# Kernel optimization log

Hardware: AMD Instinct MI355X
Metric: run time of the kernel (lower is better)

Reference implementation:

```python
import jax, jax.numpy as jnp
import numpy as np

HEAD_SIZE = 64
EMBED_DIM = 1024

def setup_inputs() -> dict:
    key = jax.random.key(0)
    kx, kq, kk, kv = jax.random.split(key, 4)
    B, T, C, H = 8, 2048, EMBED_DIM, HEAD_SIZE
    scale = 1.0 / np.sqrt(C)
    x = jax.random.normal(kx, (B, T, C), dtype=jnp.float32)
    # nn.Linear(C, H, bias=False): weight (H, C); store as (C, H) for x @ W
    Wq = jax.random.normal(kq, (C, H), dtype=jnp.float32) * scale
    Wk = jax.random.normal(kk, (C, H), dtype=jnp.float32) * scale
    Wv = jax.random.normal(kv, (C, H), dtype=jnp.float32) * scale
    return {"x": x, "Wq": Wq, "Wk": Wk, "Wv": Wv}

def reference(x, Wq, Wk, Wv):
    B, T, C = x.shape
    H = Wq.shape[1]
    q = x @ Wq  # (B, T, H)
    k = x @ Wk
    v = x @ Wv
    # scaled scores with causal mask (tril)
    wei = jnp.einsum('bth,bsh->bts', q, k) * (H ** -0.5)  # (B, T, T)
    causal = jnp.tril(jnp.ones((T, T), dtype=bool))
    wei = jnp.where(causal, wei, -jnp.inf)
    wei = jax.nn.softmax(wei, axis=-1)
    out = jnp.einsum('bts,bsh->bth', wei, v)  # (B, T, H)
    return out
```

## Files before the change

kernel.cpp:

```cpp
#include <hip/hip_runtime.h>

#define T_SEQ 2048
#define C_DIM 1024
#define H_DIM 64
#define B_DIM 8
#define NROW (B_DIM * T_SEQ)

typedef __attribute__((ext_vector_type(8))) short short8;
typedef __attribute__((ext_vector_type(4))) float f32x4;

__device__ __forceinline__ short f2bf(float f) {
  unsigned u = __builtin_bit_cast(unsigned, f);
  u += 0x7fffu + ((u >> 16) & 1u);
  return (short)(u >> 16);
}

__global__ __launch_bounds__(256) void w_prep(
    const float* __restrict__ Wq, const float* __restrict__ Wk,
    const float* __restrict__ Wv, short* __restrict__ Wt2) {
  const int unit = blockIdx.x * 256 + threadIdx.x;
  const int lane = unit & 63;
  const int t = unit >> 6;
  const int kh = t & 3;
  const int g = t >> 2;
  const int ntg = g % 12;
  const int kc = g / 12;
  const int n16 = lane & 15, quad = lane >> 4;
  const int mat = ntg >> 2;
  const int h = (ntg & 3) * 16 + n16;
  const int kb = kc * 128 + kh * 32 + quad * 8;
  const float* W = (mat == 0) ? Wq : (mat == 1 ? Wk : Wv);
  short8 v;
#pragma unroll
  for (int e = 0; e < 8; ++e) v[e] = f2bf(W[(size_t)(kb + e) * H_DIM + h]);
  *(short8*)(Wt2 + (size_t)unit * 8) = v;
}

__device__ __forceinline__ int lds_addr(int tile, int kh, int qd, int nn) {
  return tile * 2048 + kh * 512 + (qd * 16 + (nn ^ ((kh * 4 + qd) & 7))) * 8;
}

__global__ __launch_bounds__(256, 2) void qkv_gemm(
    const float* __restrict__ x, const short* __restrict__ Wt2,
    short* __restrict__ q, short* __restrict__ k, short* __restrict__ vt) {
  __shared__ __align__(16) short As[2][4096];
  const int tid = threadIdx.x;
  const int w = tid >> 6, lane = tid & 63;
  const int n16 = lane & 15, quad = lane >> 4;
  const int row0 = blockIdx.x * 32;

  f32x4 acc[2][3];
#pragma unroll
  for (int mt = 0; mt < 2; ++mt)
#pragma unroll
    for (int ln = 0; ln < 3; ++ln) acc[mt][ln] = (f32x4){0.f, 0.f, 0.f, 0.f};

  const int u20 = tid, u21 = 256 + tid;
  const int sr0 = u20 >> 4, f0 = u20 & 15;
  const int sr1 = u21 >> 4, f1 = u21 & 15;
  const float* ap0 = x + (size_t)(row0 + sr0) * C_DIM + f0 * 8;
  const float* ap1 = x + (size_t)(row0 + sr1) * C_DIM + f1 * 8;
  const int soff0 = lds_addr(sr0 >> 4, f0 >> 2, f0 & 3, sr0 & 15);
  const int soff1 = lds_addr(sr1 >> 4, f1 >> 2, f1 & 3, sr1 & 15);

  int swz[4];
#pragma unroll
  for (int kh = 0; kh < 4; ++kh)
    swz[kh] = (quad * 16 + (n16 ^ ((kh * 4 + quad) & 7))) * 8;

  const short* bbase = Wt2 + (size_t)(w * 3) * 2048 + (size_t)lane * 8;

  float4 astg[2][4];
  short8 bfr[12];

#define STAGE_A(d, p)                                      \
  {                                                        \
    short8 av0, av1;                                       \
    _Pragma("unroll") for (int e = 0; e < 4; ++e) {        \
      av0[e] = f2bf(((const float*)&astg[d][0])[e]);       \
      av0[e + 4] = f2bf(((const float*)&astg[d][1])[e]);   \
      av1[e] = f2bf(((const float*)&astg[d][2])[e]);       \
      av1[e + 4] = f2bf(((const float*)&astg[d][3])[e]);   \
    }                                                      \
    *(short8*)(&As[p][0] + soff0) = av0;                   \
    *(short8*)(&As[p][0] + soff1) = av1;                   \
  }

  astg[0][0] = *(const float4*)(ap0);
  astg[0][1] = *(const float4*)(ap0 + 4);
  astg[0][2] = *(const float4*)(ap1);
  astg[0][3] = *(const float4*)(ap1 + 4);
  astg[1][0] = *(const float4*)(ap0 + 128);
  astg[1][1] = *(const float4*)(ap0 + 132);
  astg[1][2] = *(const float4*)(ap1 + 128);
  astg[1][3] = *(const float4*)(ap1 + 132);
#pragma unroll
  for (int ln = 0; ln < 3; ++ln)
#pragma unroll
    for (int kh = 0; kh < 4; ++kh)
      bfr[ln * 4 + kh] = *(const short8*)(bbase + ln * 2048 + kh * 512);
  STAGE_A(0, 0);
  asm volatile("s_waitcnt lgkmcnt(0)" ::: "memory");
  __builtin_amdgcn_sched_barrier(0);
  __builtin_amdgcn_s_barrier();
  __builtin_amdgcn_sched_barrier(0);

#pragma unroll
  for (int kc = 0; kc < 8; ++kc) {
    const short* asb = &As[kc & 1][0];
#pragma unroll
    for (int kh = 0; kh < 4; ++kh) {
      const short8 a0 = *(const short8*)(asb + kh * 512 + swz[kh]);
      const short8 a1 = *(const short8*)(asb + 2048 + kh * 512 + swz[kh]);
#pragma unroll
      for (int ln = 0; ln < 3; ++ln) {
        acc[0][ln] = __builtin_amdgcn_mfma_f32_16x16x32_bf16(
            a0, bfr[ln * 4 + kh], acc[0][ln], 0, 0, 0);
        acc[1][ln] = __builtin_amdgcn_mfma_f32_16x16x32_bf16(
            a1, bfr[ln * 4 + kh], acc[1][ln], 0, 0, 0);
      }
    }
    if (kc < 7) {
      const short* bc = bbase + (size_t)(kc + 1) * 24576;
#pragma unroll
      for (int ln = 0; ln < 3; ++ln)
#pragma unroll
        for (int kh = 0; kh < 4; ++kh)
          bfr[ln * 4 + kh] = *(const short8*)(bc + ln * 2048 + kh * 512);
      if (kc < 6) {
        astg[kc & 1][0] = *(const float4*)(ap0 + (kc + 2) * 128);
        astg[kc & 1][1] = *(const float4*)(ap0 + (kc + 2) * 128 + 4);
        astg[kc & 1][2] = *(const float4*)(ap1 + (kc + 2) * 128);
        astg[kc & 1][3] = *(const float4*)(ap1 + (kc + 2) * 128 + 4);
      }
      STAGE_A((kc + 1) & 1, (kc + 1) & 1);
      asm volatile("s_waitcnt lgkmcnt(0)" ::: "memory");
      __builtin_amdgcn_sched_barrier(0);
      __builtin_amdgcn_s_barrier();
      __builtin_amdgcn_sched_barrier(0);
    }
  }
#undef STAGE_A

  const int b = row0 >> 11;
#pragma unroll
  for (int mt = 0; mt < 2; ++mt)
#pragma unroll
    for (int ln = 0; ln < 3; ++ln) {
      const int ntg = w * 3 + ln;
      const int mat = ntg >> 2;
      const int cl = (ntg & 3) * 16 + n16;
#pragma unroll
      for (int r = 0; r < 4; ++r) {
        const int row = row0 + mt * 16 + quad * 4 + r;
        const float v = acc[mt][ln][r];
        if (mat == 0)
          q[(size_t)row * H_DIM + cl] = f2bf(v * 0.125f);
        else if (mat == 1)
          k[(size_t)row * H_DIM + cl] = f2bf(v);
        else
          vt[((size_t)b * H_DIM + cl) * T_SEQ + (row & (T_SEQ - 1))] = f2bf(v);
      }
    }
}

__global__ __launch_bounds__(256) void attn_mfma(
    const short* __restrict__ q, const short* __restrict__ k,
    const short* __restrict__ vt, float* __restrict__ out) {
  __shared__ __align__(16) short pbuf[4][2048];
  __shared__ __align__(16) float oshare[3][2048];
  __shared__ __align__(16) float lshare[3][512];
  const int tid = threadIdx.x;
  const int w = tid >> 6;
  const int lane = tid & 63;
  const int n16 = lane & 15, quad = lane >> 4;
  const int b = blockIdx.x & 7;
  const int pa = blockIdx.x >> 3;
  const int r0a = pa * 16;
  const int r0b = (127 - pa) * 16;

  const short* kb = k + (size_t)b * T_SEQ * H_DIM;
  const short* vb = vt + (size_t)b * H_DIM * T_SEQ;
  const short* qpa = q + ((size_t)b * T_SEQ + r0a) * H_DIM;
  const short* qpb = q + ((size_t)b * T_SEQ + r0b) * H_DIM;

  short8 aqA[2], aqB[2];
  aqA[0] = *(const short8*)(qpa + (size_t)n16 * H_DIM + quad * 8);
  aqA[1] = *(const short8*)(qpa + (size_t)n16 * H_DIM + 32 + quad * 8);
  aqB[0] = *(const short8*)(qpb + (size_t)n16 * H_DIM + quad * 8);
  aqB[1] = *(const short8*)(qpb + (size_t)n16 * H_DIM + 32 + quad * 8);

  f32x4 OA[4], OB[4];
#pragma unroll
  for (int i = 0; i < 4; ++i) {
    OA[i] = (f32x4){0.f, 0.f, 0.f, 0.f};
    OB[i] = (f32x4){0.f, 0.f, 0.f, 0.f};
  }
  float lsA[4] = {0.f, 0.f, 0.f, 0.f};
  float lsB[4] = {0.f, 0.f, 0.f, 0.f};

  const int nj = (r0b + 16 + 63) >> 6;
  const int njA = (r0a + 16 + 63) >> 6;

  for (int jt = w; jt < nj; jt += 4) {
    const int j0 = jt * 64;
    const bool actA = (jt < njA);

    short8 bk[4][2];
#pragma unroll
    for (int nt = 0; nt < 4; ++nt) {
      const short* kp = kb + (size_t)(j0 + nt * 16 + n16) * H_DIM + quad * 8;
      bk[nt][0] = *(const short8*)kp;
      bk[nt][1] = *(const short8*)(kp + 32);
    }

    f32x4 sB[4];
#pragma unroll
    for (int nt = 0; nt < 4; ++nt) {
      f32x4 z = (f32x4){0.f, 0.f, 0.f, 0.f};
      z = __builtin_amdgcn_mfma_f32_16x16x32_bf16(aqB[0], bk[nt][0], z, 0, 0, 0);
      z = __builtin_amdgcn_mfma_f32_16x16x32_bf16(aqB[1], bk[nt][1], z, 0, 0, 0);
      sB[nt] = z;
    }
    f32x4 sA[4];
    if (actA) {
#pragma unroll
      for (int nt = 0; nt < 4; ++nt) {
        f32x4 z = (f32x4){0.f, 0.f, 0.f, 0.f};
        z = __builtin_amdgcn_mfma_f32_16x16x32_bf16(aqA[0], bk[nt][0], z, 0, 0, 0);
        z = __builtin_amdgcn_mfma_f32_16x16x32_bf16(aqA[1], bk[nt][1], z, 0, 0, 0);
        sA[nt] = z;
      }
    }

    const bool fullB = (j0 + 64 <= r0b);
#pragma unroll
    for (int nt = 0; nt < 4; ++nt) {
      const int base =
          (nt >> 1) * 512 + ((((nt & 1) << 1) | (n16 >> 3)) * 128) + (n16 & 7);
#pragma unroll
      for (int r = 0; r < 4; ++r) {
        float p;
        if (fullB) {
          p = __expf(sB[nt][r]);
        } else {
          const int j = j0 + nt * 16 + n16;
          const int row = r0b + quad * 4 + r;
          p = (j <= row) ? __expf(sB[nt][r]) : 0.f;
        }
        lsB[r] += p;
        pbuf[w][1024 + base + (quad * 4 + r) * 8] = f2bf(p);
      }
    }
    if (actA) {
      const bool fullA = (j0 + 64 <= r0a);
#pragma unroll
      for (int nt = 0; nt < 4; ++nt) {
        const int base =
            (nt >> 1) * 512 + ((((nt & 1) << 1) | (n16 >> 3)) * 128) + (n16 & 7);
#pragma unroll
        for (int r = 0; r < 4; ++r) {
          float p;
          if (fullA) {
            p = __expf(sA[nt][r]);
          } else {
            const int j = j0 + nt * 16 + n16;
            const int row = r0a + quad * 4 + r;
            p = (j <= row) ? __expf(sA[nt][r]) : 0.f;
          }
          lsA[r] += p;
          pbuf[w][base + (quad * 4 + r) * 8] = f2bf(p);
        }
      }
    }

    short8 bv[4][2];
#pragma unroll
    for (int ht = 0; ht < 4; ++ht)
#pragma unroll
      for (int kh = 0; kh < 2; ++kh)
        bv[ht][kh] = *(const short8*)(vb + (size_t)(ht * 16 + n16) * T_SEQ +
                                      j0 + kh * 32 + quad * 8);

    const short8 apB0 = *(const short8*)(&pbuf[w][1024] + lane * 8);
    const short8 apB1 = *(const short8*)(&pbuf[w][1536] + lane * 8);
#pragma unroll
    for (int ht = 0; ht < 4; ++ht) {
      OB[ht] = __builtin_amdgcn_mfma_f32_16x16x32_bf16(apB0, bv[ht][0], OB[ht], 0, 0, 0);
      OB[ht] = __builtin_amdgcn_mfma_f32_16x16x32_bf16(apB1, bv[ht][1], OB[ht], 0, 0, 0);
    }
    if (actA) {
      const short8 apA0 = *(const short8*)(&pbuf[w][0] + lane * 8);
      const short8 apA1 = *(const short8*)(&pbuf[w][512] + lane * 8);
#pragma unroll
      for (int ht = 0; ht < 4; ++ht) {
        OA[ht] = __builtin_amdgcn_mfma_f32_16x16x32_bf16(apA0, bv[ht][0], OA[ht], 0, 0, 0);
        OA[ht] = __builtin_amdgcn_mfma_f32_16x16x32_bf16(apA1, bv[ht][1], OA[ht], 0, 0, 0);
      }
    }
  }

  if (w != 0) {
#pragma unroll
    for (int ht = 0; ht < 4; ++ht)
#pragma unroll
      for (int r = 0; r < 4; ++r) {
        oshare[w - 1][(ht * 4 + r) * 64 + lane] = OA[ht][r];
        oshare[w - 1][1024 + (ht * 4 + r) * 64 + lane] = OB[ht][r];
      }
#pragma unroll
    for (int r = 0; r < 4; ++r) {
      lshare[w - 1][r * 64 + lane] = lsA[r];
      lshare[w - 1][256 + r * 64 + lane] = lsB[r];
    }
  }
  __syncthreads();
  if (w == 0) {
#pragma unroll
    for (int ht = 0; ht < 4; ++ht)
#pragma unroll
      for (int r = 0; r < 4; ++r) {
        float a = OA[ht][r], bb = OB[ht][r];
#pragma unroll
        for (int ow = 0; ow < 3; ++ow) {
          a += oshare[ow][(ht * 4 + r) * 64 + lane];
          bb += oshare[ow][1024 + (ht * 4 + r) * 64 + lane];
        }
        OA[ht][r] = a;
        OB[ht][r] = bb;
      }
#pragma unroll
    for (int r = 0; r < 4; ++r) {
      float va = lsA[r], vb2 = lsB[r];
#pragma unroll
      for (int ow = 0; ow < 3; ++ow) {
        va += lshare[ow][r * 64 + lane];
        vb2 += lshare[ow][256 + r * 64 + lane];
      }
      va += __shfl_xor(va, 1);
      va += __shfl_xor(va, 2);
      va += __shfl_xor(va, 4);
      va += __shfl_xor(va, 8);
      vb2 += __shfl_xor(vb2, 1);
      vb2 += __shfl_xor(vb2, 2);
      vb2 += __shfl_xor(vb2, 4);
      vb2 += __shfl_xor(vb2, 8);
      lsA[r] = va;
      lsB[r] = vb2;
    }
#pragma unroll
    for (int ht = 0; ht < 4; ++ht)
#pragma unroll
      for (int r = 0; r < 4; ++r) {
        out[((size_t)b * T_SEQ + r0a + quad * 4 + r) * H_DIM + ht * 16 + n16] =
            OA[ht][r] / lsA[r];
        out[((size_t)b * T_SEQ + r0b + quad * 4 + r) * H_DIM + ht * 16 + n16] =
            OB[ht][r] / lsB[r];
      }
  }
}

extern "C" void kernel_launch(void* const* d_in, const int* in_sizes, int n_in,
                              void* d_out, int out_size, void* d_ws,
                              size_t ws_size, hipStream_t stream) {
  const float* x = (const float*)d_in[0];
  const float* Wq = (const float*)d_in[1];
  const float* Wk = (const float*)d_in[2];
  const float* Wv = (const float*)d_in[3];

  char* ws = (char*)d_ws;
  short* Wt = (short*)ws;
  short* q = (short*)(ws + 3 * 64 * 1024 * 2);
  short* kk = (short*)(ws + 3 * 64 * 1024 * 2 + 2097152);
  short* vt = (short*)(ws + 3 * 64 * 1024 * 2 + 2 * 2097152);

  w_prep<<<96, 256, 0, stream>>>(Wq, Wk, Wv, Wt);
  qkv_gemm<<<NROW / 32, 256, 0, stream>>>(x, Wt, q, kk, vt);
  attn_mfma<<<B_DIM * (T_SEQ / 32), 256, 0, stream>>>(q, kk, vt, (float*)d_out);
}
```

Measured before the change: 137.0 us.

## Double-buffer K/V register loads across key tiles in attention loop

Restructures the per-wave key-tile loop to prefetch the next tile's K and V fragments into a second register set while the current tile's QK MFMAs and softmax run. The loop is manually unrolled by two with ping-pong buffers, and launch_bounds now requests 2 blocks per CU. The aim is to hide global load latency behind compute. It doubles the register footprint for K/V fragments, which the occupancy hint may force into spills.

```diff
diff --git a/kernel.cpp b/kernel.cpp
--- a/kernel.cpp
+++ b/kernel.cpp
@@ -164,7 +164,7 @@
     }
 }
 
-__global__ __launch_bounds__(256) void attn_mfma(
+__global__ __launch_bounds__(256, 2) void attn_mfma(
     const short* __restrict__ q, const short* __restrict__ k,
     const short* __restrict__ vt, float* __restrict__ out) {
   __shared__ __align__(16) short pbuf[4][2048];
@@ -202,103 +202,115 @@
   const int nj = (r0b + 16 + 63) >> 6;
   const int njA = (r0a + 16 + 63) >> 6;
 
-  for (int jt = w; jt < nj; jt += 4) {
-    const int j0 = jt * 64;
-    const bool actA = (jt < njA);
-
-    short8 bk[4][2];
-#pragma unroll
-    for (int nt = 0; nt < 4; ++nt) {
-      const short* kp = kb + (size_t)(j0 + nt * 16 + n16) * H_DIM + quad * 8;
-      bk[nt][0] = *(const short8*)kp;
-      bk[nt][1] = *(const short8*)(kp + 32);
-    }
-
-    f32x4 sB[4];
-#pragma unroll
-    for (int nt = 0; nt < 4; ++nt) {
-      f32x4 z = (f32x4){0.f, 0.f, 0.f, 0.f};
-      z = __builtin_amdgcn_mfma_f32_16x16x32_bf16(aqB[0], bk[nt][0], z, 0, 0, 0);
-      z = __builtin_amdgcn_mfma_f32_16x16x32_bf16(aqB[1], bk[nt][1], z, 0, 0, 0);
-      sB[nt] = z;
-    }
-    f32x4 sA[4];
-    if (actA) {
-#pragma unroll
-      for (int nt = 0; nt < 4; ++nt) {
-        f32x4 z = (f32x4){0.f, 0.f, 0.f, 0.f};
-        z = __builtin_amdgcn_mfma_f32_16x16x32_bf16(aqA[0], bk[nt][0], z, 0, 0, 0);
-        z = __builtin_amdgcn_mfma_f32_16x16x32_bf16(aqA[1], bk[nt][1], z, 0, 0, 0);
-        sA[nt] = z;
-      }
-    }
-
-    const bool fullB = (j0 + 64 <= r0b);
-#pragma unroll
-    for (int nt = 0; nt < 4; ++nt) {
-      const int base =
-          (nt >> 1) * 512 + ((((nt & 1) << 1) | (n16 >> 3)) * 128) + (n16 & 7);
-#pragma unroll
-      for (int r = 0; r < 4; ++r) {
-        float p;
-        if (fullB) {
-          p = __expf(sB[nt][r]);
-        } else {
-          const int j = j0 + nt * 16 + n16;
-          const int row = r0b + quad * 4 + r;
-          p = (j <= row) ? __expf(sB[nt][r]) : 0.f;
-        }
-        lsB[r] += p;
-        pbuf[w][1024 + base + (quad * 4 + r) * 8] = f2bf(p);
-      }
-    }
-    if (actA) {
-      const bool fullA = (j0 + 64 <= r0a);
-#pragma unroll
-      for (int nt = 0; nt < 4; ++nt) {
-        const int base =
-            (nt >> 1) * 512 + ((((nt & 1) << 1) | (n16 >> 3)) * 128) + (n16 & 7);
-#pragma unroll
-        for (int r = 0; r < 4; ++r) {
-          float p;
-          if (fullA) {
-            p = __expf(sA[nt][r]);
-          } else {
-            const int j = j0 + nt * 16 + n16;
-            const int row = r0a + quad * 4 + r;
-            p = (j <= row) ? __expf(sA[nt][r]) : 0.f;
-          }
-          lsA[r] += p;
-          pbuf[w][base + (quad * 4 + r) * 8] = f2bf(p);
-        }
-      }
-    }
-
-    short8 bv[4][2];
-#pragma unroll
-    for (int ht = 0; ht < 4; ++ht)
-#pragma unroll
-      for (int kh = 0; kh < 2; ++kh)
-        bv[ht][kh] = *(const short8*)(vb + (size_t)(ht * 16 + n16) * T_SEQ +
-                                      j0 + kh * 32 + quad * 8);
-
-    const short8 apB0 = *(const short8*)(&pbuf[w][1024] + lane * 8);
-    const short8 apB1 = *(const short8*)(&pbuf[w][1536] + lane * 8);
-#pragma unroll
-    for (int ht = 0; ht < 4; ++ht) {
-      OB[ht] = __builtin_amdgcn_mfma_f32_16x16x32_bf16(apB0, bv[ht][0], OB[ht], 0, 0, 0);
-      OB[ht] = __builtin_amdgcn_mfma_f32_16x16x32_bf16(apB1, bv[ht][1], OB[ht], 0, 0, 0);
-    }
-    if (actA) {
-      const short8 apA0 = *(const short8*)(&pbuf[w][0] + lane * 8);
-      const short8 apA1 = *(const short8*)(&pbuf[w][512] + lane * 8);
-#pragma unroll
-      for (int ht = 0; ht < 4; ++ht) {
-        OA[ht] = __builtin_amdgcn_mfma_f32_16x16x32_bf16(apA0, bv[ht][0], OA[ht], 0, 0, 0);
-        OA[ht] = __builtin_amdgcn_mfma_f32_16x16x32_bf16(apA1, bv[ht][1], OA[ht], 0, 0, 0);
-      }
-    }
-  }
+  short8 bk0[4][2], bv0[4][2], bk1[4][2], bv1[4][2];
+
+#define LOADK(BK, J0)                                                        \
+  _Pragma("unroll") for (int nt = 0; nt < 4; ++nt) {                         \
+    const short* kp = kb + (size_t)((J0) + nt * 16 + n16) * H_DIM + quad * 8; \
+    BK[nt][0] = *(const short8*)kp;                                          \
+    BK[nt][1] = *(const short8*)(kp + 32);                                   \
+  }
+#define LOADV(BV, J0)                                                        \
+  _Pragma("unroll") for (int ht = 0; ht < 4; ++ht)                           \
+  _Pragma("unroll") for (int kh = 0; kh < 2; ++kh)                           \
+      BV[ht][kh] = *(const short8*)(vb + (size_t)(ht * 16 + n16) * T_SEQ +   \
+                                    (J0) + kh * 32 + quad * 8);
+
+#define DOITER(BK, BV, JT, ...)                                               \
+  {                                                                           \
+    const int j0 = (JT) * 64;                                                 \
+    const bool actA = ((JT) < njA);                                           \
+    f32x4 sB[4];                                                              \
+    _Pragma("unroll") for (int nt = 0; nt < 4; ++nt) {                        \
+      f32x4 z = (f32x4){0.f, 0.f, 0.f, 0.f};                                  \
+      z = __builtin_amdgcn_mfma_f32_16x16x32_bf16(aqB[0], BK[nt][0], z, 0, 0, 0); \
+      z = __builtin_amdgcn_mfma_f32_16x16x32_bf16(aqB[1], BK[nt][1], z, 0, 0, 0); \
+      sB[nt] = z;                                                             \
+    }                                                                         \
+    f32x4 sA[4];                                                              \
+    if (actA) {                                                               \
+      _Pragma("unroll") for (int nt = 0; nt < 4; ++nt) {                      \
+        f32x4 z = (f32x4){0.f, 0.f, 0.f, 0.f};                                \
+        z = __builtin_amdgcn_mfma_f32_16x16x32_bf16(aqA[0], BK[nt][0], z, 0, 0, 0); \
+        z = __builtin_amdgcn_mfma_f32_16x16x32_bf16(aqA[1], BK[nt][1], z, 0, 0, 0); \
+        sA[nt] = z;                                                           \
+      }                                                                       \
+    }                                                                         \
+    __VA_ARGS__     \
+    const bool fullB = (j0 + 64 <= r0b);                                      \
+    _Pragma("unroll") for (int nt = 0; nt < 4; ++nt) {                        \
+      const int base = (nt >> 1) * 512 +                                      \
+                       ((((nt & 1) << 1) | (n16 >> 3)) * 128) + (n16 & 7);    \
+      _Pragma("unroll") for (int r = 0; r < 4; ++r) {                         \
+        float p;                                                              \
+        if (fullB) {                                                          \
+          p = __expf(sB[nt][r]);                                              \
+        } else {                                                              \
+          const int j = j0 + nt * 16 + n16;                                   \
+          const int row = r0b + quad * 4 + r;                                 \
+          p = (j <= row) ? __expf(sB[nt][r]) : 0.f;                           \
+        }                                                                     \
+        lsB[r] += p;                                                          \
+        pbuf[w][1024 + base + (quad * 4 + r) * 8] = f2bf(p);                  \
+      }                                                                       \
+    }                                                                         \
+    if (actA) {                                                               \
+      const bool fullA = (j0 + 64 <= r0a);                                    \
+      _Pragma("unroll") for (int nt = 0; nt < 4; ++nt) {                      \
+        const int base = (nt >> 1) * 512 +                                    \
+                         ((((nt & 1) << 1) | (n16 >> 3)) * 128) + (n16 & 7);  \
+        _Pragma("unroll") for (int r = 0; r < 4; ++r) {                       \
+          float p;                                                            \
+          if (fullA) {                                                        \
+            p = __expf(sA[nt][r]);                                            \
+          } else {                                                            \
+            const int j = j0 + nt * 16 + n16;                                 \
+            const int row = r0a + quad * 4 + r;                               \
+            p = (j <= row) ? __expf(sA[nt][r]) : 0.f;                         \
+          }                                                                   \
+          lsA[r] += p;                                                        \
+          pbuf[w][base + (quad * 4 + r) * 8] = f2bf(p);                       \
+        }                                                                     \
+      }                                                                       \
+    }                                                                         \
+    const short8 apB0 = *(const short8*)(&pbuf[w][1024] + lane * 8);          \
+    const short8 apB1 = *(const short8*)(&pbuf[w][1536] + lane * 8);          \
+    _Pragma("unroll") for (int ht = 0; ht < 4; ++ht) {                        \
+      OB[ht] = __builtin_amdgcn_mfma_f32_16x16x32_bf16(apB0, BV[ht][0], OB[ht], 0, 0, 0); \
+      OB[ht] = __builtin_amdgcn_mfma_f32_16x16x32_bf16(apB1, BV[ht][1], OB[ht], 0, 0, 0); \
+    }                                                                         \
+    if (actA) {                                                               \
+      const short8 apA0 = *(const short8*)(&pbuf[w][0] + lane * 8);           \
+      const short8 apA1 = *(const short8*)(&pbuf[w][512] + lane * 8);         \
+      _Pragma("unroll") for (int ht = 0; ht < 4; ++ht) {                      \
+        OA[ht] = __builtin_amdgcn_mfma_f32_16x16x32_bf16(apA0, BV[ht][0], OA[ht], 0, 0, 0); \
+        OA[ht] = __builtin_amdgcn_mfma_f32_16x16x32_bf16(apA1, BV[ht][1], OA[ht], 0, 0, 0); \
+      }                                                                       \
+    }                                                                         \
+  }
+
+  {
+    const int j00 = w * 64;
+    LOADK(bk0, j00);
+    LOADV(bv0, j00);
+  }
+  for (int jt = w; jt < nj; jt += 8) {
+    const int jB = jt + 4;
+    DOITER(bk0, bv0, jt, if (jB < nj) {
+      LOADK(bk1, jB * 64);
+      LOADV(bv1, jB * 64);
+    })
+    if (jB < nj) {
+      const int jC = jt + 8;
+      DOITER(bk1, bv1, jB, if (jC < nj) {
+        LOADK(bk0, jC * 64);
+        LOADV(bv0, jC * 64);
+      })
+    }
+  }
+#undef DOITER
+#undef LOADK
+#undef LOADV
 
   if (w != 0) {
 #pragma unroll
```

Result: slower. 148.5 us (+8.4%).

## Split attention KV loop across single-wave blocks with global partial combine kernel

Applied to the files above, without the earlier changes.

Replaces the 4-wave attention block, which reduced partials through shared memory, with 64-thread blocks. Each block handles one of 6 strided KV phases for a query tile pair, and the launch grows to 3072 blocks. Unnormalized partial outputs and row sums go to a global workspace, and a new combine kernel sums them and normalizes. The aim is more parallelism and occupancy, and less shared memory and block-level sync. The cost is an extra kernel launch plus about 25 MB of partial-result writes and reads through global memory. The V loads are also moved earlier in the loop to overlap with the score MFMAs.

```diff
diff --git a/kernel.cpp b/kernel.cpp
--- a/kernel.cpp
+++ b/kernel.cpp
@@ -5,6 +5,7 @@
 #define H_DIM 64
 #define B_DIM 8
 #define NROW (B_DIM * T_SEQ)
+#define PH 6
 
 typedef __attribute__((ext_vector_type(8))) short short8;
 typedef __attribute__((ext_vector_type(4))) float f32x4;
@@ -164,18 +165,17 @@
     }
 }
 
-__global__ __launch_bounds__(256) void attn_mfma(
+__global__ __launch_bounds__(64, 3) void attn_part(
     const short* __restrict__ q, const short* __restrict__ k,
-    const short* __restrict__ vt, float* __restrict__ out) {
-  __shared__ __align__(16) short pbuf[4][2048];
-  __shared__ __align__(16) float oshare[3][2048];
-  __shared__ __align__(16) float lshare[3][512];
-  const int tid = threadIdx.x;
-  const int w = tid >> 6;
-  const int lane = tid & 63;
+    const short* __restrict__ vt, float* __restrict__ Opart,
+    float* __restrict__ lpart) {
+  __shared__ __align__(16) short pbuf[2048];
+  const int lane = threadIdx.x;
   const int n16 = lane & 15, quad = lane >> 4;
-  const int b = blockIdx.x & 7;
-  const int pa = blockIdx.x >> 3;
+  const int blk = blockIdx.x;
+  const int b = blk & 7;
+  const int ph = (blk >> 3) % PH;
+  const int pa = blk / (8 * PH);
   const int r0a = pa * 16;
   const int r0b = (127 - pa) * 16;
 
@@ -199,10 +199,10 @@
   float lsA[4] = {0.f, 0.f, 0.f, 0.f};
   float lsB[4] = {0.f, 0.f, 0.f, 0.f};
 
-  const int nj = (r0b + 16 + 63) >> 6;
-  const int njA = (r0a + 16 + 63) >> 6;
-
-  for (int jt = w; jt < nj; jt += 4) {
+  const int nj = (r0b + 79) >> 6;
+  const int njA = (r0a + 79) >> 6;
+
+  for (int jt = ph; jt < nj; jt += PH) {
     const int j0 = jt * 64;
     const bool actA = (jt < njA);
 
@@ -213,6 +213,13 @@
       bk[nt][0] = *(const short8*)kp;
       bk[nt][1] = *(const short8*)(kp + 32);
     }
+    short8 bv[4][2];
+#pragma unroll
+    for (int ht = 0; ht < 4; ++ht)
+#pragma unroll
+      for (int kh = 0; kh < 2; ++kh)
+        bv[ht][kh] = *(const short8*)(vb + (size_t)(ht * 16 + n16) * T_SEQ +
+                                      j0 + kh * 32 + quad * 8);
 
     f32x4 sB[4];
 #pragma unroll
@@ -222,17 +229,6 @@
       z = __builtin_amdgcn_mfma_f32_16x16x32_bf16(aqB[1], bk[nt][1], z, 0, 0, 0);
       sB[nt] = z;
     }
-    f32x4 sA[4];
-    if (actA) {
-#pragma unroll
-      for (int nt = 0; nt < 4; ++nt) {
-        f32x4 z = (f32x4){0.f, 0.f, 0.f, 0.f};
-        z = __builtin_amdgcn_mfma_f32_16x16x32_bf16(aqA[0], bk[nt][0], z, 0, 0, 0);
-        z = __builtin_amdgcn_mfma_f32_16x16x32_bf16(aqA[1], bk[nt][1], z, 0, 0, 0);
-        sA[nt] = z;
-      }
-    }
-
     const bool fullB = (j0 + 64 <= r0b);
 #pragma unroll
     for (int nt = 0; nt < 4; ++nt) {
@@ -249,10 +245,19 @@
           p = (j <= row) ? __expf(sB[nt][r]) : 0.f;
         }
         lsB[r] += p;
-        pbuf[w][1024 + base + (quad * 4 + r) * 8] = f2bf(p);
-      }
-    }
+        pbuf[1024 + base + (quad * 4 + r) * 8] = f2bf(p);
+      }
+    }
+
     if (actA) {
+      f32x4 sA[4];
+#pragma unroll
+      for (int nt = 0; nt < 4; ++nt) {
+        f32x4 z = (f32x4){0.f, 0.f, 0.f, 0.f};
+        z = __builtin_amdgcn_mfma_f32_16x16x32_bf16(aqA[0], bk[nt][0], z, 0, 0, 0);
+        z = __builtin_amdgcn_mfma_f32_16x16x32_bf16(aqA[1], bk[nt][1], z, 0, 0, 0);
+        sA[nt] = z;
+      }
       const bool fullA = (j0 + 64 <= r0a);
 #pragma unroll
       for (int nt = 0; nt < 4; ++nt) {
@@ -269,29 +274,21 @@
             p = (j <= row) ? __expf(sA[nt][r]) : 0.f;
           }
           lsA[r] += p;
-          pbuf[w][base + (quad * 4 + r) * 8] = f2bf(p);
+          pbuf[base + (quad * 4 + r) * 8] = f2bf(p);
         }
       }
     }
 
-    short8 bv[4][2];
-#pragma unroll
-    for (int ht = 0; ht < 4; ++ht)
-#pragma unroll
-      for (int kh = 0; kh < 2; ++kh)
-        bv[ht][kh] = *(const short8*)(vb + (size_t)(ht * 16 + n16) * T_SEQ +
-                                      j0 + kh * 32 + quad * 8);
-
-    const short8 apB0 = *(const short8*)(&pbuf[w][1024] + lane * 8);
-    const short8 apB1 = *(const short8*)(&pbuf[w][1536] + lane * 8);
+    const short8 apB0 = *(const short8*)(&pbuf[1024] + lane * 8);
+    const short8 apB1 = *(const short8*)(&pbuf[1536] + lane * 8);
 #pragma unroll
     for (int ht = 0; ht < 4; ++ht) {
       OB[ht] = __builtin_amdgcn_mfma_f32_16x16x32_bf16(apB0, bv[ht][0], OB[ht], 0, 0, 0);
       OB[ht] = __builtin_amdgcn_mfma_f32_16x16x32_bf16(apB1, bv[ht][1], OB[ht], 0, 0, 0);
     }
     if (actA) {
-      const short8 apA0 = *(const short8*)(&pbuf[w][0] + lane * 8);
-      const short8 apA1 = *(const short8*)(&pbuf[w][512] + lane * 8);
+      const short8 apA0 = *(const short8*)(&pbuf[0] + lane * 8);
+      const short8 apA1 = *(const short8*)(&pbuf[512] + lane * 8);
 #pragma unroll
       for (int ht = 0; ht < 4; ++ht) {
         OA[ht] = __builtin_amdgcn_mfma_f32_16x16x32_bf16(apA0, bv[ht][0], OA[ht], 0, 0, 0);
@@ -300,63 +297,75 @@
     }
   }
 
-  if (w != 0) {
-#pragma unroll
-    for (int ht = 0; ht < 4; ++ht)
-#pragma unroll
-      for (int r = 0; r < 4; ++r) {
-        oshare[w - 1][(ht * 4 + r) * 64 + lane] = OA[ht][r];
-        oshare[w - 1][1024 + (ht * 4 + r) * 64 + lane] = OB[ht][r];
-      }
+#pragma unroll
+  for (int r = 0; r < 4; ++r) {
+    float va = lsA[r], vb2 = lsB[r];
+    va += __shfl_xor(va, 1);
+    va += __shfl_xor(va, 2);
+    va += __shfl_xor(va, 4);
+    va += __shfl_xor(va, 8);
+    vb2 += __shfl_xor(vb2, 1);
+    vb2 += __shfl_xor(vb2, 2);
+    vb2 += __shfl_xor(vb2, 4);
+    vb2 += __shfl_xor(vb2, 8);
+    lsA[r] = va;
+    lsB[r] = vb2;
+  }
+
+  float* opA = Opart + (size_t)blk * 2048;
+  float* opB = opA + 1024;
+#pragma unroll
+  for (int ht = 0; ht < 4; ++ht)
 #pragma unroll
     for (int r = 0; r < 4; ++r) {
-      lshare[w - 1][r * 64 + lane] = lsA[r];
-      lshare[w - 1][256 + r * 64 + lane] = lsB[r];
-    }
-  }
-  __syncthreads();
-  if (w == 0) {
-#pragma unroll
-    for (int ht = 0; ht < 4; ++ht)
-#pragma unroll
-      for (int r = 0; r < 4; ++r) {
-        float a = OA[ht][r], bb = OB[ht][r];
-#pragma unroll
-        for (int ow = 0; ow < 3; ++ow) {
-          a += oshare[ow][(ht * 4 + r) * 64 + lane];
-          bb += oshare[ow][1024 + (ht * 4 + r) * 64 + lane];
-        }
-        OA[ht][r] = a;
-        OB[ht][r] = bb;
-      }
+      opA[(ht * 4 + r) * 64 + lane] = OA[ht][r];
+      opB[(ht * 4 + r) * 64 + lane] = OB[ht][r];
+    }
+  if (n16 == 0) {
 #pragma unroll
     for (int r = 0; r < 4; ++r) {
-      float va = lsA[r], vb2 = lsB[r];
-#pragma unroll
-      for (int ow = 0; ow < 3; ++ow) {
-        va += lshare[ow][r * 64 + lane];
-        vb2 += lshare[ow][256 + r * 64 + lane];
-      }
-      va += __shfl_xor(va, 1);
-      va += __shfl_xor(va, 2);
-      va += __shfl_xor(va, 4);
-      va += __shfl_xor(va, 8);
-      vb2 += __shfl_xor(vb2, 1);
-      vb2 += __shfl_xor(vb2, 2);
-      vb2 += __shfl_xor(vb2, 4);
-      vb2 += __shfl_xor(vb2, 8);
-      lsA[r] = va;
-      lsB[r] = vb2;
-    }
-#pragma unroll
-    for (int ht = 0; ht < 4; ++ht)
-#pragma unroll
-      for (int r = 0; r < 4; ++r) {
-        out[((size_t)b * T_SEQ + r0a + quad * 4 + r) * H_DIM + ht * 16 + n16] =
-            OA[ht][r] / lsA[r];
-        out[((size_t)b * T_SEQ + r0b + quad * 4 + r) * H_DIM + ht * 16 + n16] =
-            OB[ht][r] / lsB[r];
-      }
+      lpart[blk * 32 + quad * 4 + r] = lsA[r];
+      lpart[blk * 32 + 16 + quad * 4 + r] = lsB[r];
+    }
+  }
+}
+
+__global__ __launch_bounds__(128) void attn_comb(
+    const float* __restrict__ Opart, const float* __restrict__ lpart,
+    float* __restrict__ out) {
+  const int tid = threadIdx.x;
+  const int lane = tid & 63;
+  const int half = tid >> 6;
+  const int n16 = lane & 15, quad = lane >> 4;
+  const int blk = blockIdx.x;
+  const int b = blk & 7;
+  const int tile = (blk >> 3) & 1;
+  const int pa = blk >> 4;
+  const int qt = tile ? (127 - pa) : pa;
+  const int r0 = qt * 16;
+
+  float acc[8];
+#pragma unroll
+  for (int u = 0; u < 8; ++u) acc[u] = 0.f;
+  float ls[4] = {0.f, 0.f, 0.f, 0.f};
+
+#pragma unroll
+  for (int p2 = 0; p2 < PH; ++p2) {
+    const int pblk = (pa * PH + p2) * 8 + b;
+    const float* op =
+        Opart + (size_t)pblk * 2048 + tile * 1024 + half * 512;
+#pragma unroll
+    for (int u = 0; u < 8; ++u) acc[u] += op[u * 64 + lane];
+    const float* lp = lpart + pblk * 32 + tile * 16;
+#pragma unroll
+    for (int r = 0; r < 4; ++r) ls[r] += lp[quad * 4 + r];
+  }
+
+#pragma unroll
+  for (int u = 0; u < 8; ++u) {
+    const int ht = half * 2 + (u >> 2), r = u & 3;
+    out[((size_t)b * T_SEQ + r0 + quad * 4 + r) * H_DIM + ht * 16 + n16] =
+        acc[u] / ls[r];
   }
 }
 
@@ -370,11 +379,14 @@
 
   char* ws = (char*)d_ws;
   short* Wt = (short*)ws;
-  short* q = (short*)(ws + 3 * 64 * 1024 * 2);
-  short* kk = (short*)(ws + 3 * 64 * 1024 * 2 + 2097152);
-  short* vt = (short*)(ws + 3 * 64 * 1024 * 2 + 2 * 2097152);
+  short* q = (short*)(ws + 393216);
+  short* kk = (short*)(ws + 393216 + 2097152);
+  short* vt = (short*)(ws + 393216 + 2 * 2097152);
+  float* Opart = (float*)(ws + 6684672);
+  float* lpart = (float*)(ws + 6684672 + 25165824);
 
   w_prep<<<96, 256, 0, stream>>>(Wq, Wk, Wv, Wt);
   qkv_gemm<<<NROW / 32, 256, 0, stream>>>(x, Wt, q, kk, vt);
-  attn_mfma<<<B_DIM * (T_SEQ / 32), 256, 0, stream>>>(q, kk, vt, (float*)d_out);
-}
+  attn_part<<<64 * PH * 8, 64, 0, stream>>>(q, kk, vt, Opart, lpart);
+  attn_comb<<<64 * 2 * 8, 128, 0, stream>>>(Opart, lpart, (float*)d_out);
+}
```

New measurement: 143.3 us. 1.05x slower.

## Transpose S MFMA and pass P through cross-lane shuffles instead of LDS

Applied to the files above, without the earlier changes.

The QK^T MFMA operands are swapped, so each lane holds score values along the key dimension for one query row. The exponentiated probabilities are packed to bf16 with v_cvt_pk_bf16_f32 and rearranged into the PV A-operand layout with __shfl_xor exchanges, which removes the per-wave LDS P buffer and its scattered 2-byte stores. Row sums are now kept as one per-lane scalar and redistributed with shuffles at the end. This cuts LDS traffic and frees shared memory, at the cost of extra shuffle and select instructions in the inner loop. The tricky lane-permutation logic is a correctness risk.

```diff
diff --git a/kernel.cpp b/kernel.cpp
--- a/kernel.cpp
+++ b/kernel.cpp
@@ -8,11 +8,18 @@
 
 typedef __attribute__((ext_vector_type(8))) short short8;
 typedef __attribute__((ext_vector_type(4))) float f32x4;
+typedef __attribute__((ext_vector_type(4))) int i32x4;
 
 __device__ __forceinline__ short f2bf(float f) {
   unsigned u = __builtin_bit_cast(unsigned, f);
   u += 0x7fffu + ((u >> 16) & 1u);
   return (short)(u >> 16);
+}
+
+__device__ __forceinline__ unsigned pk_bf16(float lo, float hi) {
+  unsigned r;
+  asm("v_cvt_pk_bf16_f32 %0, %1, %2" : "=v"(r) : "v"(lo), "v"(hi));
+  return r;
 }
 
 __global__ __launch_bounds__(256) void w_prep(
@@ -167,7 +174,6 @@
 __global__ __launch_bounds__(256) void attn_mfma(
     const short* __restrict__ q, const short* __restrict__ k,
     const short* __restrict__ vt, float* __restrict__ out) {
-  __shared__ __align__(16) short pbuf[4][2048];
   __shared__ __align__(16) float oshare[3][2048];
   __shared__ __align__(16) float lshare[3][512];
   const int tid = threadIdx.x;
@@ -196,8 +202,7 @@
     OA[i] = (f32x4){0.f, 0.f, 0.f, 0.f};
     OB[i] = (f32x4){0.f, 0.f, 0.f, 0.f};
   }
-  float lsA[4] = {0.f, 0.f, 0.f, 0.f};
-  float lsB[4] = {0.f, 0.f, 0.f, 0.f};
+  float lsAsc = 0.f, lsBsc = 0.f;
 
   const int nj = (r0b + 16 + 63) >> 6;
   const int njA = (r0a + 16 + 63) >> 6;
@@ -218,8 +223,8 @@
 #pragma unroll
     for (int nt = 0; nt < 4; ++nt) {
       f32x4 z = (f32x4){0.f, 0.f, 0.f, 0.f};
-      z = __builtin_amdgcn_mfma_f32_16x16x32_bf16(aqB[0], bk[nt][0], z, 0, 0, 0);
-      z = __builtin_amdgcn_mfma_f32_16x16x32_bf16(aqB[1], bk[nt][1], z, 0, 0, 0);
+      z = __builtin_amdgcn_mfma_f32_16x16x32_bf16(bk[nt][0], aqB[0], z, 0, 0, 0);
+      z = __builtin_amdgcn_mfma_f32_16x16x32_bf16(bk[nt][1], aqB[1], z, 0, 0, 0);
       sB[nt] = z;
     }
     f32x4 sA[4];
@@ -227,50 +232,47 @@
 #pragma unroll
       for (int nt = 0; nt < 4; ++nt) {
         f32x4 z = (f32x4){0.f, 0.f, 0.f, 0.f};
-        z = __builtin_amdgcn_mfma_f32_16x16x32_bf16(aqA[0], bk[nt][0], z, 0, 0, 0);
-        z = __builtin_amdgcn_mfma_f32_16x16x32_bf16(aqA[1], bk[nt][1], z, 0, 0, 0);
+        z = __builtin_amdgcn_mfma_f32_16x16x32_bf16(bk[nt][0], aqA[0], z, 0, 0, 0);
+        z = __builtin_amdgcn_mfma_f32_16x16x32_bf16(bk[nt][1], aqA[1], z, 0, 0, 0);
         sA[nt] = z;
       }
     }
 
+    unsigned wB[4][2], wA[4][2];
     const bool fullB = (j0 + 64 <= r0b);
 #pragma unroll
     for (int nt = 0; nt < 4; ++nt) {
-      const int base =
-          (nt >> 1) * 512 + ((((nt & 1) << 1) | (n16 >> 3)) * 128) + (n16 & 7);
+      float p[4];
 #pragma unroll
       for (int r = 0; r < 4; ++r) {
-        float p;
         if (fullB) {
-          p = __expf(sB[nt][r]);
+          p[r] = __expf(sB[nt][r]);
         } else {
-          const int j = j0 + nt * 16 + n16;
-          const int row = r0b + quad * 4 + r;
-          p = (j <= row) ? __expf(sB[nt][r]) : 0.f;
+          const int j = j0 + nt * 16 + quad * 4 + r;
+          p[r] = (j <= r0b + n16) ? __expf(sB[nt][r]) : 0.f;
         }
-        lsB[r] += p;
-        pbuf[w][1024 + base + (quad * 4 + r) * 8] = f2bf(p);
-      }
+        lsBsc += p[r];
+      }
+      wB[nt][0] = pk_bf16(p[0], p[1]);
+      wB[nt][1] = pk_bf16(p[2], p[3]);
     }
     if (actA) {
       const bool fullA = (j0 + 64 <= r0a);
 #pragma unroll
       for (int nt = 0; nt < 4; ++nt) {
-        const int base =
-            (nt >> 1) * 512 + ((((nt & 1) << 1) | (n16 >> 3)) * 128) + (n16 & 7);
+        float p[4];
 #pragma unroll
         for (int r = 0; r < 4; ++r) {
-          float p;
           if (fullA) {
-            p = __expf(sA[nt][r]);
+            p[r] = __expf(sA[nt][r]);
           } else {
-            const int j = j0 + nt * 16 + n16;
-            const int row = r0a + quad * 4 + r;
-            p = (j <= row) ? __expf(sA[nt][r]) : 0.f;
+            const int j = j0 + nt * 16 + quad * 4 + r;
+            p[r] = (j <= r0a + n16) ? __expf(sA[nt][r]) : 0.f;
           }
-          lsA[r] += p;
-          pbuf[w][base + (quad * 4 + r) * 8] = f2bf(p);
+          lsAsc += p[r];
         }
+        wA[nt][0] = pk_bf16(p[0], p[1]);
+        wA[nt][1] = pk_bf16(p[2], p[3]);
       }
     }
 
@@ -282,22 +284,57 @@
         bv[ht][kh] = *(const short8*)(vb + (size_t)(ht * 16 + n16) * T_SEQ +
                                       j0 + kh * 32 + quad * 8);
 
-    const short8 apB0 = *(const short8*)(&pbuf[w][1024] + lane * 8);
-    const short8 apB1 = *(const short8*)(&pbuf[w][1536] + lane * 8);
+#define EXCHANGE(WSRC, AP0, AP1)                                          \
+  {                                                                       \
+    i32x4 apw[2];                                                         \
+    _Pragma("unroll") for (int h = 0; h < 2; ++h) {                       \
+      _Pragma("unroll") for (int ww = 0; ww < 2; ++ww) {                  \
+        const unsigned wlo = WSRC[2 * h][ww];                             \
+        const unsigned whi = WSRC[2 * h + 1][ww];                         \
+        const unsigned pay16 = (quad >= 2) ? whi : wlo;                   \
+        const unsigned pay2 = (quad < 2) ? whi : wlo;                     \
+        const unsigned x16 = (unsigned)__shfl_xor((int)pay16, 16);        \
+        const unsigned x32 = (unsigned)__shfl_xor((int)pay2, 32);         \
+        const unsigned x48 = (unsigned)__shfl_xor((int)pay2, 48);         \
+        const unsigned lo =                                               \
+            quad == 0 ? wlo : quad == 1 ? x48 : quad == 2 ? x32 : x16;    \
+        const unsigned hi =                                               \
+            quad == 0 ? x16 : quad == 1 ? x32 : quad == 2 ? x48 : whi;    \
+        apw[h][ww] = (int)lo;                                             \
+        apw[h][2 + ww] = (int)hi;                                         \
+      }                                                                   \
+    }                                                                     \
+    AP0 = __builtin_bit_cast(short8, apw[0]);                             \
+    AP1 = __builtin_bit_cast(short8, apw[1]);                             \
+  }
+
+    short8 apB0, apB1;
+    EXCHANGE(wB, apB0, apB1);
 #pragma unroll
     for (int ht = 0; ht < 4; ++ht) {
       OB[ht] = __builtin_amdgcn_mfma_f32_16x16x32_bf16(apB0, bv[ht][0], OB[ht], 0, 0, 0);
       OB[ht] = __builtin_amdgcn_mfma_f32_16x16x32_bf16(apB1, bv[ht][1], OB[ht], 0, 0, 0);
     }
     if (actA) {
-      const short8 apA0 = *(const short8*)(&pbuf[w][0] + lane * 8);
-      const short8 apA1 = *(const short8*)(&pbuf[w][512] + lane * 8);
+      short8 apA0, apA1;
+      EXCHANGE(wA, apA0, apA1);
 #pragma unroll
       for (int ht = 0; ht < 4; ++ht) {
         OA[ht] = __builtin_amdgcn_mfma_f32_16x16x32_bf16(apA0, bv[ht][0], OA[ht], 0, 0, 0);
         OA[ht] = __builtin_amdgcn_mfma_f32_16x16x32_bf16(apA1, bv[ht][1], OA[ht], 0, 0, 0);
       }
     }
+#undef EXCHANGE
+  }
+
+  float lsA[4], lsB[4];
+#pragma unroll
+  for (int r = 0; r < 4; ++r) {
+    const int src = (n16 & 3) * 16 + quad * 4 + r;
+    const float vA = __shfl(lsAsc, src);
+    const float vB = __shfl(lsBsc, src);
+    lsA[r] = (n16 < 4) ? vA : 0.f;
+    lsB[r] = (n16 < 4) ? vB : 0.f;
   }
 
   if (w != 0) {
```

Measured after the change: 137.4 us. Within noise of the previous version (+0.3%).
